# Optimization experiments

Measured on AMD Instinct MI355X. Metric: run time of the kernel, lower is better.

Reference implementation:

```python
import math
import jax, jax.numpy as jnp
import numpy as np

HIDDEN = 2048
HEAD_DIM = 128
NUM_HEADS = 32
NUM_KV_HEADS = 8
GROUP = NUM_HEADS // NUM_KV_HEADS
B, S = 1, 2048


def setup_inputs() -> dict:
    key = jax.random.key(0)
    ks = jax.random.split(key, 9)
    scale_in = 1.0 / math.sqrt(HIDDEN)
    scale_o = 1.0 / math.sqrt(NUM_HEADS * HEAD_DIM)
    x = jax.random.normal(ks[0], (B, S, HIDDEN), dtype=jnp.float32)
    # causal mask (1,1,S,S), int32; masked positions are 0
    mask = jnp.tril(jnp.ones((S, S), dtype=jnp.int32))[None, None]
    wq = jax.random.uniform(ks[1], (HIDDEN, NUM_HEADS * HEAD_DIM), jnp.float32, -scale_in, scale_in)
    bq = jax.random.uniform(ks[2], (NUM_HEADS * HEAD_DIM,), jnp.float32, -scale_in, scale_in)
    wk = jax.random.uniform(ks[3], (HIDDEN, NUM_KV_HEADS * HEAD_DIM), jnp.float32, -scale_in, scale_in)
    bk = jax.random.uniform(ks[4], (NUM_KV_HEADS * HEAD_DIM,), jnp.float32, -scale_in, scale_in)
    wv = jax.random.uniform(ks[5], (HIDDEN, NUM_KV_HEADS * HEAD_DIM), jnp.float32, -scale_in, scale_in)
    bv = jax.random.uniform(ks[6], (NUM_KV_HEADS * HEAD_DIM,), jnp.float32, -scale_in, scale_in)
    wo = jax.random.uniform(ks[7], (NUM_HEADS * HEAD_DIM, HIDDEN), jnp.float32, -scale_o, scale_o)
    bo = jax.random.uniform(ks[8], (HIDDEN,), jnp.float32, -scale_o, scale_o)
    return {"x": x, "mask": mask, "wq": wq, "bq": bq, "wk": wk, "bk": bk,
            "wv": wv, "bv": bv, "wo": wo, "bo": bo}


def reference(x, mask, wq, bq, wk, bk, wv, bv, wo, bo):
    Bb, Ss, _ = x.shape
    inv_sqrt_d = 1.0 / math.sqrt(HEAD_DIM)
    # projections
    q = (x @ wq + bq).reshape(Bb, Ss, NUM_KV_HEADS, GROUP, HEAD_DIM)  # grouped query heads
    k = (x @ wk + bk).reshape(Bb, Ss, NUM_KV_HEADS, HEAD_DIM)
    v = (x @ wv + bv).reshape(Bb, Ss, NUM_KV_HEADS, HEAD_DIM)
    # repeat_interleave(group, dim=2) on k/v == broadcasting each kv head over its
    # GROUP consecutive query heads; einsum avoids the physical KV blow-up.
    scores = jnp.einsum('bqhgd,bshd->bhgqs', q, k) * inv_sqrt_d  # (B, Hkv, G, S, S)
    m = mask[:, :, None]  # (1,1,1,S,S) broadcasts over (Hkv, G)
    scores = jnp.where(m == 0, -jnp.inf, scores)
    attn = jax.nn.softmax(scores, axis=-1)
    out = jnp.einsum('bhgqs,bshd->bqhgd', attn, v).reshape(Bb, Ss, NUM_HEADS * HEAD_DIM)
    return out @ wo + bo
```

## Files before the change

### kernel.cpp

```cpp
#include <hip/hip_runtime.h>

#define HIDDEN 2048
#define S_LEN  2048
#define NH     32
#define NKV    8
#define HD     128
#define QKVN   6144
#define OD     4096

typedef float  f32x4   __attribute__((ext_vector_type(4)));
typedef float  f32x16  __attribute__((ext_vector_type(16)));
typedef __bf16 bf16x8  __attribute__((ext_vector_type(8)));
typedef __bf16 bf16x4  __attribute__((ext_vector_type(4)));
typedef unsigned int u32;

static __device__ __forceinline__ f32x4 mfma16(bf16x8 a, bf16x8 b, f32x4 c) {
  return __builtin_amdgcn_mfma_f32_16x16x32_bf16(a, b, c, 0, 0, 0);
}
static __device__ __forceinline__ f32x16 mfma32(bf16x8 a, bf16x8 b, f32x16 c) {
  return __builtin_amdgcn_mfma_f32_32x32x16_bf16(a, b, c, 0, 0, 0);
}
static __device__ __forceinline__ void gload_lds16(const void* g, void* l) {
  __builtin_amdgcn_global_load_lds(
      (__attribute__((address_space(1))) void*)(g),
      (__attribute__((address_space(3))) void*)(l), 16, 0, 0);
}
static __device__ __forceinline__ u32 pk_bf16(float lo, float hi) {
  u32 r;
  asm("v_cvt_pk_bf16_f32 %0, %1, %2" : "=v"(r) : "v"(lo), "v"(hi));
  return r;
}

__global__ __launch_bounds__(256) void k_cvt(const float* __restrict__ in,
                                             __bf16* __restrict__ out, int n) {
  int i = (blockIdx.x * 256 + threadIdx.x) * 4;
  if (i >= n) return;
  float4 v = *reinterpret_cast<const float4*>(in + i);
  bf16x4 o = {(__bf16)v.x, (__bf16)v.y, (__bf16)v.z, (__bf16)v.w};
  *reinterpret_cast<bf16x4*>(out + i) = o;
}

__global__ __launch_bounds__(256) void k_transpose_cvt(const float* __restrict__ src,
                                                       __bf16* __restrict__ dst,
                                                       int K, int N) {
  __shared__ float tile[32][33];
  int tx = threadIdx.x & 31, ty = threadIdx.x >> 5;
  int n0 = blockIdx.x * 32, k0 = blockIdx.y * 32;
#pragma unroll
  for (int r = 0; r < 4; r++) {
    int k = ty + r * 8;
    tile[k][tx] = src[(size_t)(k0 + k) * N + n0 + tx];
  }
  __syncthreads();
#pragma unroll
  for (int r = 0; r < 4; r++) {
    int n = ty + r * 8;
    dst[(size_t)(n0 + n) * K + k0 + tx] = (__bf16)tile[tx][n];
  }
}

__global__ void k_bias_concat(const float* __restrict__ bq, const float* __restrict__ bk,
                              const float* __restrict__ bv, float* __restrict__ out) {
  int i = blockIdx.x * 256 + threadIdx.x;
  if (i >= QKVN) return;
  out[i] = (i < 4096) ? bq[i] : (i < 5120 ? bk[i - 4096] : bv[i - 5120]);
}

__global__ __launch_bounds__(256) void k_vtrans(const __bf16* __restrict__ qkv,
                                                __bf16* __restrict__ vt) {
  __shared__ __bf16 tile[32][33];
  int tx = threadIdx.x & 31, ty = threadIdx.x >> 5;
  int s0 = blockIdx.x * 32, d0 = blockIdx.y * 32, kv = blockIdx.z;
#pragma unroll
  for (int r = 0; r < 4; r++) {
    int s = ty + r * 8;
    tile[s][tx] = qkv[(size_t)(s0 + s) * QKVN + 5120 + kv * HD + d0 + tx];
  }
  __syncthreads();
#pragma unroll
  for (int r = 0; r < 4; r++) {
    int d = ty + r * 8;
    vt[(size_t)(kv * HD + d0 + d) * S_LEN + s0 + tx] = tile[tx][d];
  }
}

__global__ __launch_bounds__(256, 2) void k_gemm8(const __bf16* __restrict__ A,
                                                  const __bf16* __restrict__ BT,
                                                  const float* __restrict__ bias,
                                                  __bf16* __restrict__ C,
                                                  int M, int N, int K,
                                                  float oscale, int scale_cols) {
  __shared__ __bf16 Al[2][2][4096];
  __shared__ __bf16 Bl[2][2][6144];
  const int tid = threadIdx.x, lane = tid & 63, w = tid >> 6;
  const int l15 = lane & 15, lhi = lane >> 4;
  const int sw = ((blockIdx.x & 7) << 6) + (blockIdx.x >> 3);
  const int mt = sw & 15, nt = sw >> 4;
  const int m0 = mt * 128, n0 = nt * 192;
  const int NKT = K >> 6;
  const __bf16* Ab = A + (size_t)m0 * K;
  const __bf16* Bb = BT + (size_t)n0 * K;

  f32x4 acc[8][3];
#pragma unroll
  for (int i = 0; i < 8; i++)
#pragma unroll
    for (int j = 0; j < 3; j++)
#pragma unroll
      for (int e = 0; e < 4; e++) acc[i][j][e] = 0.f;

#define SGH(buf, kh, ktile)                                                       \
  do {                                                                            \
    _Pragma("unroll") for (int it = 0; it < 2; ++it) {                            \
      int c = it * 256 + tid;                                                     \
      int row = c >> 2, slot = c & 3;                                             \
      int scol = ((slot * 16) ^ (((row >> 1) & 3) << 4)) >> 1;                    \
      gload_lds16(Ab + (size_t)row * K + (ktile) * 64 + (kh) * 32 + scol,         \
                  &Al[buf][kh][c * 8]);                                           \
    }                                                                             \
    _Pragma("unroll") for (int it = 0; it < 3; ++it) {                            \
      int c = it * 256 + tid;                                                     \
      int row = c >> 2, slot = c & 3;                                             \
      int scol = ((slot * 16) ^ (((row >> 1) & 3) << 4)) >> 1;                    \
      gload_lds16(Bb + (size_t)row * K + (ktile) * 64 + (kh) * 32 + scol,         \
                  &Bl[buf][kh][c * 8]);                                           \
    }                                                                             \
  } while (0)

#define RD_AB(cb, kk)                                                             \
  do {                                                                            \
    _Pragma("unroll") for (int i = 0; i < 8; ++i) {                               \
      int row = i * 16 + l15;                                                     \
      af[i] = *(const bf16x8*)(&Al[cb][kk][row * 32 +                             \
                (((lhi * 16) ^ (((row >> 1) & 3) << 4)) >> 1)]);                  \
    }                                                                             \
    _Pragma("unroll") for (int j = 0; j < 3; ++j) {                               \
      int row = w * 48 + j * 16 + l15;                                            \
      bfr[j] = *(const bf16x8*)(&Bl[cb][kk][row * 32 +                            \
                (((lhi * 16) ^ (((row >> 1) & 3) << 4)) >> 1)]);                  \
    }                                                                             \
  } while (0)

#define MFMA24X                                                                   \
  do {                                                                            \
    __builtin_amdgcn_s_setprio(1);                                                \
    _Pragma("unroll") for (int i = 0; i < 8; ++i) {                               \
      _Pragma("unroll") for (int j = 0; j < 3; ++j) {                             \
        acc[i][j] = mfma16(af[i], bfr[j], acc[i][j]);                             \
      }                                                                           \
    }                                                                             \
    __builtin_amdgcn_s_setprio(0);                                                \
  } while (0)

  SGH(0, 0, 0);
  SGH(0, 1, 0);
  asm volatile("s_waitcnt vmcnt(5)" ::: "memory");
  __builtin_amdgcn_s_barrier();
  __builtin_amdgcn_sched_barrier(0);

  for (int kt = 0; kt < NKT; ++kt) {
    const int cb = kt & 1, pb = cb ^ 1;
    const bool pf = (kt + 1 < NKT);
    bf16x8 af[8], bfr[3];

    RD_AB(cb, 0);
    if (pf) SGH(pb, 0, kt + 1);
    __builtin_amdgcn_s_barrier();
    asm volatile("s_waitcnt lgkmcnt(0)" ::: "memory");
    MFMA24X;
    if (pf) {
      asm volatile("s_waitcnt vmcnt(5)" ::: "memory");
    } else {
      asm volatile("s_waitcnt vmcnt(0)" ::: "memory");
    }
    __builtin_amdgcn_s_barrier();
    __builtin_amdgcn_sched_barrier(0);

    RD_AB(cb, 1);
    if (pf) SGH(pb, 1, kt + 1);
    __builtin_amdgcn_s_barrier();
    asm volatile("s_waitcnt lgkmcnt(0)" ::: "memory");
    MFMA24X;
    if (pf) {
      asm volatile("s_waitcnt vmcnt(5)" ::: "memory");
    }
    __builtin_amdgcn_s_barrier();
    __builtin_amdgcn_sched_barrier(0);
  }
#undef SGH
#undef RD_AB
#undef MFMA24X

#pragma unroll
  for (int j = 0; j < 3; j++) {
    int col = n0 + w * 48 + j * 16 + l15;
    float bv = bias[col];
    float sc = (col < scale_cols) ? oscale : 1.0f;
#pragma unroll
    for (int i = 0; i < 8; i++) {
      int r0 = m0 + i * 16 + lhi * 4;
#pragma unroll
      for (int rr = 0; rr < 4; rr++) {
        C[(size_t)(r0 + rr) * N + col] = (__bf16)((acc[i][j][rr] + bv) * sc);
      }
    }
  }
}

__global__ __launch_bounds__(256) void k_gemm_part(const __bf16* __restrict__ A,
                                                   const __bf16* __restrict__ BT,
                                                   float* __restrict__ Cpart,
                                                   int M, int N, int K, int KC) {
  __shared__ __bf16 Al[128 * 64];
  __shared__ __bf16 Bl[128 * 64];
  const int tid = threadIdx.x;
  const int lane = tid & 63;
  const int w = tid >> 6;
  const int m0 = blockIdx.y * 128;
  const int n0 = blockIdx.x * 128;
  const int kbeg = blockIdx.z * KC;
  const int wm = (w >> 1) * 64;
  const int wn = (w & 1) * 64;
  const int l15 = lane & 15, lhi = lane >> 4;

  f32x4 acc[4][4];
#pragma unroll
  for (int i = 0; i < 4; i++)
#pragma unroll
    for (int j = 0; j < 4; j++)
#pragma unroll
      for (int e = 0; e < 4; e++) acc[i][j][e] = 0.f;

  for (int kt = kbeg; kt < kbeg + KC; kt += 64) {
#pragma unroll
    for (int it = 0; it < 4; it++) {
      int idx = it * 256 + tid;
      int row = idx >> 3, slot = idx & 7;
      int scol = ((slot * 16) ^ ((row & 7) << 4)) >> 1;
      gload_lds16(A + (size_t)(m0 + row) * K + kt + scol, &Al[idx * 8]);
      gload_lds16(BT + (size_t)(n0 + row) * K + kt + scol, &Bl[idx * 8]);
    }
    __syncthreads();
#pragma unroll
    for (int kk = 0; kk < 2; kk++) {
      bf16x8 af[4], bfr[4];
#pragma unroll
      for (int i = 0; i < 4; i++) {
        int ra = wm + i * 16 + l15;
        int ba = (kk * 64 + lhi * 16) ^ ((ra & 7) << 4);
        af[i] = *(const bf16x8*)((const char*)Al + ra * 128 + ba);
        int rb = wn + i * 16 + l15;
        int bb = (kk * 64 + lhi * 16) ^ ((rb & 7) << 4);
        bfr[i] = *(const bf16x8*)((const char*)Bl + rb * 128 + bb);
      }
#pragma unroll
      for (int i = 0; i < 4; i++)
#pragma unroll
        for (int j = 0; j < 4; j++) acc[i][j] = mfma16(af[i], bfr[j], acc[i][j]);
    }
    __syncthreads();
  }
  float* C = Cpart + (size_t)blockIdx.z * M * N;
#pragma unroll
  for (int j = 0; j < 4; j++) {
    int col = n0 + wn + j * 16 + l15;
#pragma unroll
    for (int i = 0; i < 4; i++) {
      int r0 = m0 + wm + i * 16 + lhi * 4;
#pragma unroll
      for (int rr = 0; rr < 4; rr++) {
        C[(size_t)(r0 + rr) * N + col] = acc[i][j][rr];
      }
    }
  }
}

__global__ __launch_bounds__(256) void k_ocombine(const float* __restrict__ a,
                                                  const float* __restrict__ b,
                                                  const float* __restrict__ bias,
                                                  float* __restrict__ out) {
  int i = (blockIdx.x * 256 + threadIdx.x) * 4;
  f32x4 va = *(const f32x4*)(a + i);
  f32x4 vb = *(const f32x4*)(b + i);
  f32x4 vbias = *(const f32x4*)(bias + (i & (HIDDEN - 1)));
  f32x4 r = va + vb + vbias;
  *(f32x4*)(out + i) = r;
}

__global__ __launch_bounds__(256, 2) void k_attn(const __bf16* __restrict__ qkv,
                                                 const __bf16* __restrict__ vt,
                                                 __bf16* __restrict__ o) {
  __shared__ __bf16 Kl[2][8192];
  __shared__ __bf16 Vl[2][8192];
  const int tid = threadIdx.x, lane = tid & 63, w = tid >> 6;
  const int l31 = lane & 31, h = lane >> 5;

  const int id = blockIdx.x;
  int tile, head;
  if (id < 256) { head = id >> 4; tile = id & 15; }
  else          { head = 16 + ((id - 256) >> 4); tile = 15 - (id & 15); }
  const int kvh = head >> 2;
  const int qbase = tile * 128 + w * 32;
  const int qg = qbase + l31;
  const int kdiag = (qbase + 31) >> 6;
  const int nkt = 2 * tile + 2;

  bf16x8 qf[8];
  {
    const __bf16* qrow = qkv + (size_t)qg * QKVN + head * HD;
#pragma unroll
    for (int dk = 0; dk < 8; dk++) qf[dk] = *(const bf16x8*)(qrow + dk * 16 + h * 8);
  }

  f32x16 acc[4];
#pragma unroll
  for (int dt = 0; dt < 4; dt++)
#pragma unroll
    for (int r = 0; r < 16; r++) acc[dt][r] = 0.f;
  float m = -INFINITY, lsum = 0.f;

#define STAGE(buf, ktile)                                                           \
  do {                                                                              \
    const int kk0 = (ktile) * 64;                                                   \
    _Pragma("unroll") for (int it = 0; it < 4; it++) {                              \
      int c = it * 256 + tid;                                                       \
      int key = c >> 4, slot = c & 15;                                              \
      int scol = ((slot * 16) ^ ((key & 15) << 4)) >> 1;                            \
      gload_lds16(qkv + (size_t)(kk0 + key) * QKVN + 4096 + kvh * HD + scol,        \
                  &Kl[buf][c * 8]);                                                 \
    }                                                                               \
    _Pragma("unroll") for (int it = 0; it < 4; it++) {                              \
      int c = it * 256 + tid;                                                       \
      int d = c >> 3, slot = c & 7;                                                 \
      int scol = ((slot * 16) ^ ((d & 7) << 4)) >> 1;                               \
      gload_lds16(vt + (size_t)(kvh * HD + d) * S_LEN + kk0 + scol,                 \
                  &Vl[buf][c * 8]);                                                 \
    }                                                                               \
  } while (0)

  STAGE(0, 0);
  __syncthreads();

  for (int kt = 0; kt < nkt; kt++) {
    const int cur = kt & 1;
    if (kt + 1 < nkt) STAGE(cur ^ 1, kt + 1);

    if (kt <= kdiag) {
      const char* Kb = (const char*)&Kl[cur][0];
      const char* Vb = (const char*)&Vl[cur][0];
      const int k0 = kt * 64;
      f32x16 sacc[2];
#pragma unroll
      for (int b = 0; b < 2; b++)
#pragma unroll
        for (int r = 0; r < 16; r++) sacc[b][r] = 0.f;
      __builtin_amdgcn_s_setprio(1);
#pragma unroll
      for (int dk = 0; dk < 8; dk++) {
        const int sA = ((2 * dk + h) ^ (l31 & 15)) * 16;
        bf16x8 kf0 = *(const bf16x8*)(Kb + l31 * 256 + sA);
        bf16x8 kf1 = *(const bf16x8*)(Kb + (32 + l31) * 256 + sA);
        sacc[0] = mfma32(kf0, qf[dk], sacc[0]);
        sacc[1] = mfma32(kf1, qf[dk], sacc[1]);
      }
      __builtin_amdgcn_s_setprio(0);
      float p[32];
#pragma unroll
      for (int b = 0; b < 2; b++)
#pragma unroll
        for (int r = 0; r < 16; r++) p[b * 16 + r] = sacc[b][r];
      if (kt == kdiag) {
#pragma unroll
        for (int b = 0; b < 2; b++)
#pragma unroll
          for (int r = 0; r < 16; r++) {
            int keyg = k0 + b * 32 + (r & 3) + 8 * (r >> 2) + 4 * h;
            if (keyg > qg) p[b * 16 + r] = -INFINITY;
          }
      }
      float t16[16], t8[8], t4[4];
#pragma unroll
      for (int i = 0; i < 16; i++) t16[i] = fmaxf(p[2 * i], p[2 * i + 1]);
#pragma unroll
      for (int i = 0; i < 8; i++) t8[i] = fmaxf(t16[2 * i], t16[2 * i + 1]);
#pragma unroll
      for (int i = 0; i < 4; i++) t4[i] = fmaxf(t8[2 * i], t8[2 * i + 1]);
      float pm = fmaxf(fmaxf(t4[0], t4[1]), fmaxf(t4[2], t4[3]));
      pm = fmaxf(pm, __shfl_xor(pm, 32));
      if (__any(pm - m > 8.f)) {
        float mn = fmaxf(m, pm);
        float corr = __expf(m - mn);
        m = mn;
        lsum *= corr;
#pragma unroll
        for (int dt = 0; dt < 4; dt++)
#pragma unroll
          for (int r = 0; r < 16; r++) acc[dt][r] *= corr;
      }
      float psum = 0.f;
#pragma unroll
      for (int i = 0; i < 32; i++) { p[i] = __expf(p[i] - m); psum += p[i]; }
      lsum += psum;
#pragma unroll
      for (int ks2 = 0; ks2 < 4; ks2++) {
        const int o8 = (ks2 >> 1) * 16 + (ks2 & 1) * 8;
        u32 W0 = pk_bf16(p[o8 + 0], p[o8 + 1]);
        u32 W1 = pk_bf16(p[o8 + 2], p[o8 + 3]);
        u32 W2 = pk_bf16(p[o8 + 4], p[o8 + 5]);
        u32 W3 = pk_bf16(p[o8 + 6], p[o8 + 7]);
        asm("v_permlane32_swap_b32 %0, %1" : "+v"(W0), "+v"(W2));
        asm("v_permlane32_swap_b32 %0, %1" : "+v"(W1), "+v"(W3));
        union { u32 wd[4]; bf16x8 v; } pu;
        pu.wd[0] = W0; pu.wd[1] = W1; pu.wd[2] = W2; pu.wd[3] = W3;
        __builtin_amdgcn_s_setprio(1);
#pragma unroll
        for (int dt = 0; dt < 4; dt++) {
          const int dr = dt * 32 + l31;
          const int sV = ((2 * ks2 + h) ^ (dr & 7)) * 16;
          bf16x8 vf = *(const bf16x8*)(Vb + dr * 128 + sV);
          acc[dt] = mfma32(vf, pu.v, acc[dt]);
        }
        __builtin_amdgcn_s_setprio(0);
      }
    }
    __syncthreads();
  }
#undef STAGE

  lsum += __shfl_xor(lsum, 32);
  const float inv = 1.f / lsum;
  __bf16* orow = o + (size_t)qg * OD + head * HD;
#pragma unroll
  for (int dt = 0; dt < 4; dt++)
#pragma unroll
    for (int rq = 0; rq < 4; rq++) {
      int d = dt * 32 + 8 * rq + 4 * h;
      bf16x4 ov = {(__bf16)(acc[dt][rq * 4 + 0] * inv), (__bf16)(acc[dt][rq * 4 + 1] * inv),
                   (__bf16)(acc[dt][rq * 4 + 2] * inv), (__bf16)(acc[dt][rq * 4 + 3] * inv)};
      *(bf16x4*)(orow + d) = ov;
    }
}

extern "C" void kernel_launch(void* const* d_in, const int* in_sizes, int n_in,
                              void* d_out, int out_size, void* d_ws, size_t ws_size,
                              hipStream_t stream) {
  const float* x  = (const float*)d_in[0];
  const float* wq = (const float*)d_in[2];
  const float* bq = (const float*)d_in[3];
  const float* wk = (const float*)d_in[4];
  const float* bk = (const float*)d_in[5];
  const float* wv = (const float*)d_in[6];
  const float* bv = (const float*)d_in[7];
  const float* wo = (const float*)d_in[8];
  const float* bo = (const float*)d_in[9];
  float* out = (float*)d_out;

  const size_t MB = 1024 * 1024;
  char* ws = (char*)d_ws;
  __bf16* xb    = (__bf16*)(ws);
  __bf16* wqkvT = (__bf16*)(ws + 8 * MB);
  __bf16* woT   = (__bf16*)(ws + 32 * MB);
  __bf16* qkvb  = (__bf16*)(ws + 48 * MB);
  __bf16* vtb   = (__bf16*)(ws + 72 * MB);
  __bf16* ob    = (__bf16*)(ws + 76 * MB);
  float*  bqkv  = (float*)(ws + 92 * MB);
  float*  Cpart = (float*)(ws);

  k_cvt<<<4096, 256, 0, stream>>>(x, xb, HIDDEN * S_LEN);
  k_transpose_cvt<<<dim3(128, 64), 256, 0, stream>>>(wq, wqkvT, HIDDEN, 4096);
  k_transpose_cvt<<<dim3(32, 64), 256, 0, stream>>>(wk, wqkvT + (size_t)4096 * HIDDEN, HIDDEN, 1024);
  k_transpose_cvt<<<dim3(32, 64), 256, 0, stream>>>(wv, wqkvT + (size_t)5120 * HIDDEN, HIDDEN, 1024);
  k_transpose_cvt<<<dim3(64, 128), 256, 0, stream>>>(wo, woT, 4096, HIDDEN);
  k_bias_concat<<<24, 256, 0, stream>>>(bq, bk, bv, bqkv);

  k_gemm8<<<512, 256, 0, stream>>>(xb, wqkvT, bqkv, qkvb, S_LEN, QKVN, HIDDEN,
                                   0.08838834764831845f, 4096);
  k_vtrans<<<dim3(S_LEN / 32, HD / 32, NKV), 256, 0, stream>>>(qkvb, vtb);
  k_attn<<<512, 256, 0, stream>>>(qkvb, vtb, ob);
  k_gemm_part<<<dim3(HIDDEN / 128, S_LEN / 128, 2), 256, 0, stream>>>(
      ob, woT, Cpart, S_LEN, HIDDEN, OD, OD / 2);
  k_ocombine<<<(S_LEN * HIDDEN) / 1024, 256, 0, stream>>>(
      Cpart, Cpart + (size_t)S_LEN * HIDDEN, bo, out);
}
```

Measured before the change: 218.3 us.

## Double-buffer output-projection split-K GEMM with half-tile prefetch and swizzled block order

Rewrites the split-K output projection GEMM to double-buffer LDS in two K-halves. The next tile's global-to-LDS loads are issued while MFMAs run on the current one, using explicit waitcnt, barriers and raised setprio around the MFMA block. It also swaps the warp layout to 8x2 16x16 fragments per wave (the B fragment per wave, full 128 rows of A) and uses a swizzled 1D grid for L2 locality. This aims to hide memory latency in a kernel that used to fully synchronise each K step, but it doubles LDS use and adds register pressure.

```diff
diff --git a/kernel.cpp b/kernel.cpp
--- a/kernel.cpp
+++ b/kernel.cpp
@@ -207,66 +207,120 @@
   }
 }
 
-__global__ __launch_bounds__(256) void k_gemm_part(const __bf16* __restrict__ A,
-                                                   const __bf16* __restrict__ BT,
-                                                   float* __restrict__ Cpart,
-                                                   int M, int N, int K, int KC) {
-  __shared__ __bf16 Al[128 * 64];
-  __shared__ __bf16 Bl[128 * 64];
-  const int tid = threadIdx.x;
-  const int lane = tid & 63;
-  const int w = tid >> 6;
-  const int m0 = blockIdx.y * 128;
-  const int n0 = blockIdx.x * 128;
-  const int kbeg = blockIdx.z * KC;
-  const int wm = (w >> 1) * 64;
-  const int wn = (w & 1) * 64;
+__global__ __launch_bounds__(256, 2) void k_gemm_part(const __bf16* __restrict__ A,
+                                                      const __bf16* __restrict__ BT,
+                                                      float* __restrict__ Cpart,
+                                                      int M, int N, int K, int KC) {
+  __shared__ __bf16 Al[2][2][4096];
+  __shared__ __bf16 Bl[2][2][4096];
+  const int tid = threadIdx.x, lane = tid & 63, w = tid >> 6;
   const int l15 = lane & 15, lhi = lane >> 4;
-
-  f32x4 acc[4][4];
-#pragma unroll
-  for (int i = 0; i < 4; i++)
-#pragma unroll
-    for (int j = 0; j < 4; j++)
+  const int bid = blockIdx.x;
+  const int z = bid >> 8, rem = bid & 255;
+  const int sw = ((rem & 7) << 5) + (rem >> 3);
+  const int mt = sw & 15, nt = sw >> 4;
+  const int m0 = mt * 128, n0 = nt * 128;
+  const int NKT = KC >> 6;
+  const __bf16* Ab = A + (size_t)m0 * K + (size_t)z * KC;
+  const __bf16* Bb = BT + (size_t)n0 * K + (size_t)z * KC;
+
+  f32x4 acc[8][2];
+#pragma unroll
+  for (int i = 0; i < 8; i++)
+#pragma unroll
+    for (int j = 0; j < 2; j++)
 #pragma unroll
       for (int e = 0; e < 4; e++) acc[i][j][e] = 0.f;
 
-  for (int kt = kbeg; kt < kbeg + KC; kt += 64) {
-#pragma unroll
-    for (int it = 0; it < 4; it++) {
-      int idx = it * 256 + tid;
-      int row = idx >> 3, slot = idx & 7;
-      int scol = ((slot * 16) ^ ((row & 7) << 4)) >> 1;
-      gload_lds16(A + (size_t)(m0 + row) * K + kt + scol, &Al[idx * 8]);
-      gload_lds16(BT + (size_t)(n0 + row) * K + kt + scol, &Bl[idx * 8]);
-    }
-    __syncthreads();
-#pragma unroll
-    for (int kk = 0; kk < 2; kk++) {
-      bf16x8 af[4], bfr[4];
-#pragma unroll
-      for (int i = 0; i < 4; i++) {
-        int ra = wm + i * 16 + l15;
-        int ba = (kk * 64 + lhi * 16) ^ ((ra & 7) << 4);
-        af[i] = *(const bf16x8*)((const char*)Al + ra * 128 + ba);
-        int rb = wn + i * 16 + l15;
-        int bb = (kk * 64 + lhi * 16) ^ ((rb & 7) << 4);
-        bfr[i] = *(const bf16x8*)((const char*)Bl + rb * 128 + bb);
-      }
-#pragma unroll
-      for (int i = 0; i < 4; i++)
-#pragma unroll
-        for (int j = 0; j < 4; j++) acc[i][j] = mfma16(af[i], bfr[j], acc[i][j]);
-    }
-    __syncthreads();
-  }
-  float* C = Cpart + (size_t)blockIdx.z * M * N;
-#pragma unroll
-  for (int j = 0; j < 4; j++) {
-    int col = n0 + wn + j * 16 + l15;
-#pragma unroll
-    for (int i = 0; i < 4; i++) {
-      int r0 = m0 + wm + i * 16 + lhi * 4;
+#define SGH2(buf, kh, ktile)                                                      \
+  do {                                                                            \
+    _Pragma("unroll") for (int it = 0; it < 2; ++it) {                            \
+      int c = it * 256 + tid;                                                     \
+      int row = c >> 2, slot = c & 3;                                             \
+      int scol = ((slot * 16) ^ (((row >> 1) & 3) << 4)) >> 1;                    \
+      gload_lds16(Ab + (size_t)row * K + (ktile) * 64 + (kh) * 32 + scol,         \
+                  &Al[buf][kh][c * 8]);                                           \
+    }                                                                             \
+    _Pragma("unroll") for (int it = 0; it < 2; ++it) {                            \
+      int c = it * 256 + tid;                                                     \
+      int row = c >> 2, slot = c & 3;                                             \
+      int scol = ((slot * 16) ^ (((row >> 1) & 3) << 4)) >> 1;                    \
+      gload_lds16(Bb + (size_t)row * K + (ktile) * 64 + (kh) * 32 + scol,         \
+                  &Bl[buf][kh][c * 8]);                                           \
+    }                                                                             \
+  } while (0)
+
+#define RD_AB2(cb, kk)                                                            \
+  do {                                                                            \
+    _Pragma("unroll") for (int i = 0; i < 8; ++i) {                               \
+      int row = i * 16 + l15;                                                     \
+      af[i] = *(const bf16x8*)(&Al[cb][kk][row * 32 +                             \
+                (((lhi * 16) ^ (((row >> 1) & 3) << 4)) >> 1)]);                  \
+    }                                                                             \
+    _Pragma("unroll") for (int j = 0; j < 2; ++j) {                               \
+      int row = w * 32 + j * 16 + l15;                                            \
+      bfr[j] = *(const bf16x8*)(&Bl[cb][kk][row * 32 +                            \
+                (((lhi * 16) ^ (((row >> 1) & 3) << 4)) >> 1)]);                  \
+    }                                                                             \
+  } while (0)
+
+#define MFMA16X                                                                   \
+  do {                                                                            \
+    __builtin_amdgcn_s_setprio(1);                                                \
+    _Pragma("unroll") for (int i = 0; i < 8; ++i) {                               \
+      _Pragma("unroll") for (int j = 0; j < 2; ++j) {                             \
+        acc[i][j] = mfma16(af[i], bfr[j], acc[i][j]);                             \
+      }                                                                           \
+    }                                                                             \
+    __builtin_amdgcn_s_setprio(0);                                                \
+  } while (0)
+
+  SGH2(0, 0, 0);
+  SGH2(0, 1, 0);
+  asm volatile("s_waitcnt vmcnt(4)" ::: "memory");
+  __builtin_amdgcn_s_barrier();
+  __builtin_amdgcn_sched_barrier(0);
+
+  for (int kt = 0; kt < NKT; ++kt) {
+    const int cb = kt & 1, pb = cb ^ 1;
+    const bool pf = (kt + 1 < NKT);
+    bf16x8 af[8], bfr[2];
+
+    RD_AB2(cb, 0);
+    if (pf) SGH2(pb, 0, kt + 1);
+    __builtin_amdgcn_s_barrier();
+    asm volatile("s_waitcnt lgkmcnt(0)" ::: "memory");
+    MFMA16X;
+    if (pf) {
+      asm volatile("s_waitcnt vmcnt(4)" ::: "memory");
+    } else {
+      asm volatile("s_waitcnt vmcnt(0)" ::: "memory");
+    }
+    __builtin_amdgcn_s_barrier();
+    __builtin_amdgcn_sched_barrier(0);
+
+    RD_AB2(cb, 1);
+    if (pf) SGH2(pb, 1, kt + 1);
+    __builtin_amdgcn_s_barrier();
+    asm volatile("s_waitcnt lgkmcnt(0)" ::: "memory");
+    MFMA16X;
+    if (pf) {
+      asm volatile("s_waitcnt vmcnt(4)" ::: "memory");
+    }
+    __builtin_amdgcn_s_barrier();
+    __builtin_amdgcn_sched_barrier(0);
+  }
+#undef SGH2
+#undef RD_AB2
+#undef MFMA16X
+
+  float* C = Cpart + (size_t)z * M * N;
+#pragma unroll
+  for (int j = 0; j < 2; j++) {
+    int col = n0 + w * 32 + j * 16 + l15;
+#pragma unroll
+    for (int i = 0; i < 8; i++) {
+      int r0 = m0 + i * 16 + lhi * 4;
 #pragma unroll
       for (int rr = 0; rr < 4; rr++) {
         C[(size_t)(r0 + rr) * N + col] = acc[i][j][rr];
@@ -477,8 +531,7 @@
                                    0.08838834764831845f, 4096);
   k_vtrans<<<dim3(S_LEN / 32, HD / 32, NKV), 256, 0, stream>>>(qkvb, vtb);
   k_attn<<<512, 256, 0, stream>>>(qkvb, vtb, ob);
-  k_gemm_part<<<dim3(HIDDEN / 128, S_LEN / 128, 2), 256, 0, stream>>>(
-      ob, woT, Cpart, S_LEN, HIDDEN, OD, OD / 2);
+  k_gemm_part<<<512, 256, 0, stream>>>(ob, woT, Cpart, S_LEN, HIDDEN, OD, OD / 2);
   k_ocombine<<<(S_LEN * HIDDEN) / 1024, 256, 0, stream>>>(
       Cpart, Cpart + (size_t)S_LEN * HIDDEN, bo, out);
 }
```

New measurement: 218.2 us. Within noise of the previous version (-0.1%).
